# Optimization experiments

Measured on AMD Instinct MI355X. Metric: run time of the kernel, lower is better.

## Reference

```python
import jax, jax.numpy as jnp
import numpy as np

B, N, F_IN, F_OUT, T, K = 2, 4096, 16, 16, 12, 3


def setup_inputs() -> dict:
    key = jax.random.key(0)
    k1, k2, k3, k4 = jax.random.split(key, 4)
    x = jax.random.normal(k1, (B, N, F_IN, T), dtype=jnp.float32)
    # stacked K Chebyshev polynomial matrices T_k(L~), each (N, N)
    cheb_polynomials = jax.random.normal(k2, (K, N, N), dtype=jnp.float32) / np.sqrt(N)
    # ChebNetII interpolation table: cheb_poly_xj[j, k] = T_k evaluated at node x_j (scalar)
    cheb_poly_xj = jax.random.normal(k3, (K, K), dtype=jnp.float32)
    # learned Gamma_j parameters, each (F_in, F_out)
    Gamma = jax.random.normal(k4, (K, F_IN, F_OUT), dtype=jnp.float32) * 0.1
    return {"x": x, "cheb_polynomials": cheb_polynomials,
            "cheb_poly_xj": cheb_poly_xj, "Gamma": Gamma}


def reference(x, cheb_polynomials, cheb_poly_xj, Gamma):
    # x: (B, N, F_in, T); cheb_polynomials: (K, N, N);
    # cheb_poly_xj: (K, K) scalars; Gamma: (K, F_in, F_out)
    K_ = Gamma.shape[0]
    # lhs_k = sum_j Gamma_j * cheb_poly_xj[j, k]  -> (K, F_in, F_out); hoisted out of T loop
    lhs = jnp.einsum('jio,jk->kio', Gamma, cheb_poly_xj)
    # project features first (small contraction): (K, B, N, F_out, T)
    z = jnp.einsum('bmft,kfo->kbmot', x, lhs)
    # graph propagation: rhs[b,n,f] = sum_m x[b,m,f] * T_k[m, n]  (note T_k applied on the right)
    out = jnp.einsum('kmn,kbmot->bnot', cheb_polynomials, z)
    return jax.nn.relu((2.0 / (K_ + 1)) * out)
```

## Files before the change

### kernel.cpp

```cpp
#include <hip/hip_runtime.h>
#include <stdint.h>

typedef float    f32x2 __attribute__((ext_vector_type(2)));
typedef float    f32x4 __attribute__((ext_vector_type(4)));
typedef _Float16 f16x8 __attribute__((ext_vector_type(8)));
typedef unsigned int u32x4 __attribute__((ext_vector_type(4)));

#define NN     4096
#define KTOT   12288
#define CDIM   384
#define BN     64
#define BK     32
#define TSTEPS 384

__global__ __launch_bounds__(256) void zbuild_kernel(
    const float* __restrict__ x,
    const float* __restrict__ xj,
    const float* __restrict__ gamma,
    _Float16* __restrict__ zws)
{
  __shared__ float xs[32 * 193];
  __shared__ float lhs[768];
  const int tid = threadIdx.x;
  const int b   = blockIdx.x & 1;
  const int m0  = (blockIdx.x >> 1) << 5;

  for (int e = tid; e < 768; e += 256) {
    const int k = e >> 8, fo = e & 255;
    float s = 0.f;
#pragma unroll
    for (int j = 0; j < 3; ++j) s += gamma[j * 256 + fo] * xj[j * 3 + k];
    lhs[e] = s;
  }
  const float* xsrc = x + (size_t)(b * 4096 + m0) * 192;
  for (int q = tid; q < 1536; q += 256) {
    const int fl  = q << 2;
    const int ml  = fl / 192;
    const int off = fl - ml * 192;
    const f32x4 v = *(const f32x4*)(xsrc + fl);
#pragma unroll
    for (int r = 0; r < 4; ++r) xs[ml * 193 + off + r] = v[r];
  }
  __syncthreads();

  for (int slot = tid; slot < 512; slot += 256) {
    const int ml = slot & 31, o = slot >> 5;
    float acc[3][12];
#pragma unroll
    for (int k = 0; k < 3; ++k)
#pragma unroll
      for (int t = 0; t < 12; ++t) acc[k][t] = 0.f;

#pragma unroll
    for (int f = 0; f < 16; ++f) {
      float xv[12];
#pragma unroll
      for (int t = 0; t < 12; ++t) xv[t] = xs[ml * 193 + f * 12 + t];
#pragma unroll
      for (int k = 0; k < 3; ++k) {
        const float lf = lhs[k * 256 + f * 16 + o];
#pragma unroll
        for (int t = 0; t < 12; ++t) acc[k][t] += xv[t] * lf;
      }
    }
    const int mg = m0 + ml;
    const int cb = b * 192 + o * 12;
#pragma unroll
    for (int k = 0; k < 3; ++k)
#pragma unroll
      for (int t = 0; t < 12; ++t)
        zws[(size_t)(cb + t) * KTOT + k * 4096 + mg] = (_Float16)acc[k][t];
  }
}

__global__ __launch_bounds__(512, 4) void gemm_kernel(
    const float* __restrict__ cheb,
    const _Float16* __restrict__ zws,
    float* __restrict__ partials,
    int S, int spb)
{
  __shared__ unsigned int Bs[2][BN * BK / 2];

  const int tid  = threadIdx.x;
  const int by   = blockIdx.x % S;
  const int bx   = blockIdx.x / S;
  const int lane = tid & 63, wid = tid >> 6;
  const int l15  = lane & 15, l4 = lane >> 4;
  const int nbase = bx * BN;
  const int step0 = by * spb;
  int nsteps = TSTEPS - step0;
  if (nsteps > spb) nsteps = spb;
  if (nsteps < 0) nsteps = 0;

  f32x4 acc[3][4];
#pragma unroll
  for (int mi = 0; mi < 3; ++mi)
#pragma unroll
    for (int ni = 0; ni < 4; ++ni) acc[mi][ni] = (f32x4)(0.f);

  const int rr = tid >> 5;
  const int nn = (tid & 31) << 1;
  f32x2 b0, b1;
  auto LOADB = [&](int t) {
    const float* base = cheb + (size_t)(step0 + t) * BK * NN + nbase + nn;
    b0 = *(const f32x2*)(base + (size_t)(2 * rr)     * NN);
    b1 = *(const f32x2*)(base + (size_t)(2 * rr + 1) * NN);
  };
  auto WRITEB = [&](int buf) {
#pragma unroll
    for (int d = 0; d < 2; ++d) {
      const int n = nn + d;
      const _Float16 h0 = (_Float16)b0[d], h1 = (_Float16)b1[d];
      const uint32_t w = (uint32_t)__builtin_bit_cast(unsigned short, h0) |
                         ((uint32_t)__builtin_bit_cast(unsigned short, h1) << 16);
      const int blk = (n * 4 + (rr >> 2)) ^ ((n >> 2) & 3);
      Bs[buf][blk * 4 + (rr & 3)] = w;
    }
  };

  const char* abase = (const char*)zws +
      (size_t)(wid * 48 + l15) * (KTOT * 2) + (size_t)l4 * 16;
  auto LOADA = [&](int t, u32x4* ar) {
    const size_t kb = (size_t)(step0 + t) * (BK * 2);
#pragma unroll
    for (int mi = 0; mi < 3; ++mi)
      ar[mi] = *(const u32x4*)(abase + (size_t)mi * 16 * (KTOT * 2) + kb);
  };

  auto STEP = [&](int t, u32x4* arCur, u32x4* arNxt, int cur) {
    const bool pf = (t + 1 < nsteps);
    if (pf) LOADB(t + 1);
    f16x8 bf[4];
#pragma unroll
    for (int ni = 0; ni < 4; ++ni) {
      const int n   = ni * 16 + l15;
      const int blk = (n * 4 + l4) ^ ((n >> 2) & 3);
      bf[ni] = *(const f16x8*)&Bs[cur][blk * 4];
    }
    if (pf) LOADA(t + 1, arNxt);
#pragma unroll
    for (int mi = 0; mi < 3; ++mi) {
      const f16x8 af = __builtin_bit_cast(f16x8, arCur[mi]);
#pragma unroll
      for (int ni = 0; ni < 4; ++ni)
        acc[mi][ni] = __builtin_amdgcn_mfma_f32_16x16x32_f16(
            af, bf[ni], acc[mi][ni], 0, 0, 0);
    }
    if (pf) WRITEB(cur ^ 1);
    __syncthreads();
  };

  u32x4 arA[3], arB[3];
  if (nsteps > 0) {
    LOADB(0); WRITEB(0); LOADA(0, arA);
    __syncthreads();
    int t = 0;
    for (; t + 1 < nsteps; t += 2) {
      STEP(t,     arA, arB, t & 1);
      STEP(t + 1, arB, arA, (t + 1) & 1);
    }
    if (t < nsteps) STEP(t, arA, arB, t & 1);
  }

  float* pb = partials + (size_t)by * ((size_t)CDIM * NN);
#pragma unroll
  for (int mi = 0; mi < 3; ++mi) {
    const int c0 = wid * 48 + mi * 16 + l4 * 4;
#pragma unroll
    for (int ni = 0; ni < 4; ++ni) {
      const int n = nbase + ni * 16 + l15;
#pragma unroll
      for (int r = 0; r < 4; ++r)
        pb[(size_t)(c0 + r) * NN + n] = acc[mi][ni][r];
    }
  }
}

__global__ __launch_bounds__(256) void reduce_kernel(
    const float* __restrict__ partials, float* __restrict__ out, int S)
{
  __shared__ float T[192 * 33];
  const int tid = threadIdx.x;
  const int n0  = blockIdx.x * 32;
  const int cb  = blockIdx.y;

  for (int i = tid; i < 6144; i += 256) {
    const int c_l = i >> 5, n_l = i & 31;
    const float* p = partials + (size_t)(cb * 192 + c_l) * NN + n0 + n_l;
    float s = 0.f;
    for (int ss = 0; ss < S; ++ss) s += p[(size_t)ss * ((size_t)CDIM * NN)];
    T[c_l * 33 + n_l] = s;
  }
  __syncthreads();
  for (int j = tid; j < 6144; j += 256) {
    const int n_l = j / 192, ot = j - n_l * 192;
    const float v = 0.5f * T[ot * 33 + n_l];
    out[(size_t)(cb * 4096 + n0 + n_l) * 192 + ot] = v > 0.f ? v : 0.f;
  }
}

extern "C" void kernel_launch(void* const* d_in, const int* in_sizes, int n_in,
                              void* d_out, int out_size, void* d_ws, size_t ws_size,
                              hipStream_t stream) {
  (void)in_sizes; (void)n_in; (void)out_size;
  const float* x     = (const float*)d_in[0];
  const float* cheb  = (const float*)d_in[1];
  const float* xj    = (const float*)d_in[2];
  const float* gamma = (const float*)d_in[3];
  float* out = (float*)d_out;

  const long long zbytes = (long long)CDIM * KTOT * 2;
  const long long pslab  = (long long)CDIM * NN * 4;
  int S = 8;
  const long long avail = (long long)ws_size - zbytes;
  if (avail < 8 * pslab) {
    S = (int)(avail / pslab);
    if (S < 1) S = 1;
    if (S > 8) S = 8;
  }
  const int spb = (TSTEPS + S - 1) / S;

  _Float16* zws   = (_Float16*)d_ws;
  float* partials = (float*)((char*)d_ws + zbytes);

  zbuild_kernel<<<256, 256, 0, stream>>>(x, xj, gamma, zws);
  gemm_kernel<<<(NN / BN) * S, 512, 0, stream>>>(cheb, zws, partials, S, spb);
  reduce_kernel<<<dim3(128, 2), 256, 0, stream>>>(partials, out, S);
}
```

Measured before the change: 413.8 us.

## Deepen global prefetch to two steps and use lighter LDS-only barrier

The B tile (cheb) global loads are now issued two steps ahead using two rotating register buffers, while A still prefetches one step ahead. The __syncthreads is replaced by an explicit lgkmcnt wait plus s_barrier, so outstanding global loads (vmcnt) need not drain at each step. The LDS swizzle XOR changes from (n>>2)&3 to (n>>1)&7 to reduce bank conflicts. The aim is to hide HBM latency of the streamed fp32 matrix, at the cost of extra registers and reliance on the compiler's vmcnt handling for correctness.

```diff
diff --git a/kernel.cpp b/kernel.cpp
--- a/kernel.cpp
+++ b/kernel.cpp
@@ -100,20 +100,20 @@
 
   const int rr = tid >> 5;
   const int nn = (tid & 31) << 1;
-  f32x2 b0, b1;
-  auto LOADB = [&](int t) {
+  auto LOADB = [&](int t, f32x2* br) {
     const float* base = cheb + (size_t)(step0 + t) * BK * NN + nbase + nn;
-    b0 = *(const f32x2*)(base + (size_t)(2 * rr)     * NN);
-    b1 = *(const f32x2*)(base + (size_t)(2 * rr + 1) * NN);
-  };
-  auto WRITEB = [&](int buf) {
+    br[0] = *(const f32x2*)(base + (size_t)(2 * rr)     * NN);
+    br[1] = *(const f32x2*)(base + (size_t)(2 * rr + 1) * NN);
+  };
+  auto WRITEB = [&](int buf, f32x2* br) {
 #pragma unroll
     for (int d = 0; d < 2; ++d) {
       const int n = nn + d;
-      const _Float16 h0 = (_Float16)b0[d], h1 = (_Float16)b1[d];
+      const _Float16 h0 = (_Float16)br[0][d];
+      const _Float16 h1 = (_Float16)br[1][d];
       const uint32_t w = (uint32_t)__builtin_bit_cast(unsigned short, h0) |
                          ((uint32_t)__builtin_bit_cast(unsigned short, h1) << 16);
-      const int blk = (n * 4 + (rr >> 2)) ^ ((n >> 2) & 3);
+      const int blk = (n * 4 + (rr >> 2)) ^ ((n >> 1) & 7);
       Bs[buf][blk * 4 + (rr & 3)] = w;
     }
   };
@@ -127,39 +127,44 @@
       ar[mi] = *(const u32x4*)(abase + (size_t)mi * 16 * (KTOT * 2) + kb);
   };
 
-  auto STEP = [&](int t, u32x4* arCur, u32x4* arNxt, int cur) {
-    const bool pf = (t + 1 < nsteps);
-    if (pf) LOADB(t + 1);
+  auto STEP = [&](int t, int cur, f32x2* bL, f32x2* bW, u32x4* arC, u32x4* arN) {
+    if (t + 1 < nsteps) LOADA(t + 1, arN);
+    if (t + 2 < nsteps) LOADB(t + 2, bL);
     f16x8 bf[4];
 #pragma unroll
     for (int ni = 0; ni < 4; ++ni) {
       const int n   = ni * 16 + l15;
-      const int blk = (n * 4 + l4) ^ ((n >> 2) & 3);
+      const int blk = (n * 4 + l4) ^ ((n >> 1) & 7);
       bf[ni] = *(const f16x8*)&Bs[cur][blk * 4];
     }
-    if (pf) LOADA(t + 1, arNxt);
 #pragma unroll
     for (int mi = 0; mi < 3; ++mi) {
-      const f16x8 af = __builtin_bit_cast(f16x8, arCur[mi]);
+      const f16x8 af = __builtin_bit_cast(f16x8, arC[mi]);
 #pragma unroll
       for (int ni = 0; ni < 4; ++ni)
         acc[mi][ni] = __builtin_amdgcn_mfma_f32_16x16x32_f16(
             af, bf[ni], acc[mi][ni], 0, 0, 0);
     }
-    if (pf) WRITEB(cur ^ 1);
-    __syncthreads();
-  };
-
+    if (t + 1 < nsteps) WRITEB(cur ^ 1, bW);
+    asm volatile("s_waitcnt lgkmcnt(0)" ::: "memory");
+    __builtin_amdgcn_s_barrier();
+  };
+
+  f32x2 bs0[2], bs1[2];
   u32x4 arA[3], arB[3];
   if (nsteps > 0) {
-    LOADB(0); WRITEB(0); LOADA(0, arA);
-    __syncthreads();
+    LOADA(0, arA);
+    LOADB(0, bs0);
+    if (nsteps > 1) LOADB(1, bs1);
+    WRITEB(0, bs0);
+    asm volatile("s_waitcnt lgkmcnt(0)" ::: "memory");
+    __builtin_amdgcn_s_barrier();
     int t = 0;
     for (; t + 1 < nsteps; t += 2) {
-      STEP(t,     arA, arB, t & 1);
-      STEP(t + 1, arB, arA, (t + 1) & 1);
-    }
-    if (t < nsteps) STEP(t, arA, arB, t & 1);
+      STEP(t,     0, bs0, bs1, arA, arB);
+      STEP(t + 1, 1, bs1, bs0, arB, arA);
+    }
+    if (t < nsteps) STEP(t, 0, bs0, bs1, arA, arB);
   }
 
   float* pb = partials + (size_t)by * ((size_t)CDIM * NN);
```

Measured after the change: 411.6 us. About the same (-0.5%).

## Deepen GEMM prefetch pipeline and change LDS swizzle with manual barriers

Applied to the files above, without the earlier changes.

The GEMM main loop is rewritten with macros to prefetch the cheb (B) tiles four steps ahead and the z (A) fragments two steps ahead in rotating register sets. Each phase now writes the next LDS buffer before the MFMAs instead of after them. The LDS XOR swizzle changes from ((n>>2)&3) to ((n>>1)&7) to reduce bank conflicts. The __syncthreads is replaced by an explicit lgkmcnt wait plus s_barrier. The aim is to hide global-memory latency behind the MFMAs, at the cost of more registers under a 512-thread launch bound that allows 4 blocks.

```diff
diff --git a/kernel.cpp b/kernel.cpp
--- a/kernel.cpp
+++ b/kernel.cpp
@@ -73,6 +73,56 @@
   }
 }
 
+#define LOADA_(T, R0, R1, R2) do {                                          \
+    const size_t kb_ = (size_t)(step0 + (T)) * (BK * 2);                    \
+    R0 = *(const u32x4*)(abase + kb_);                                      \
+    R1 = *(const u32x4*)(abase + (size_t)16 * (KTOT * 2) + kb_);            \
+    R2 = *(const u32x4*)(abase + (size_t)32 * (KTOT * 2) + kb_);            \
+  } while (0)
+
+#define LOADB_(T, QA, QB) do {                                              \
+    const float* base_ = cheb + (size_t)(step0 + (T)) * BK * NN + nbase + nn; \
+    QA = *(const f32x2*)(base_ + (size_t)(2 * rr) * NN);                    \
+    QB = *(const f32x2*)(base_ + (size_t)(2 * rr + 1) * NN);                \
+  } while (0)
+
+#define WRITEB_(BUF, QA, QB) do {                                           \
+    _Float16 h0_, h1_; uint32_t w_;                                         \
+    h0_ = (_Float16)QA[0]; h1_ = (_Float16)QB[0];                           \
+    w_ = (uint32_t)__builtin_bit_cast(unsigned short, h0_) |                \
+         ((uint32_t)__builtin_bit_cast(unsigned short, h1_) << 16);         \
+    Bs[BUF][(((nn) * 4 + (rr >> 2)) ^ (((nn) >> 1) & 7)) * 4 + (rr & 3)] = w_; \
+    h0_ = (_Float16)QA[1]; h1_ = (_Float16)QB[1];                           \
+    w_ = (uint32_t)__builtin_bit_cast(unsigned short, h0_) |                \
+         ((uint32_t)__builtin_bit_cast(unsigned short, h1_) << 16);         \
+    Bs[BUF][(((nn + 1) * 4 + (rr >> 2)) ^ (((nn + 1) >> 1) & 7)) * 4 + (rr & 3)] = w_; \
+  } while (0)
+
+#define MFMA_ROW_(MI, AREG)                                                 \
+  { const f16x8 af_ = __builtin_bit_cast(f16x8, AREG);                      \
+    acc[MI][0] = __builtin_amdgcn_mfma_f32_16x16x32_f16(af_, bf0_, acc[MI][0], 0, 0, 0); \
+    acc[MI][1] = __builtin_amdgcn_mfma_f32_16x16x32_f16(af_, bf1_, acc[MI][1], 0, 0, 0); \
+    acc[MI][2] = __builtin_amdgcn_mfma_f32_16x16x32_f16(af_, bf2_, acc[MI][2], 0, 0, 0); \
+    acc[MI][3] = __builtin_amdgcn_mfma_f32_16x16x32_f16(af_, bf3_, acc[MI][3], 0, 0, 0); }
+
+#define PHASE_(T, A0_, A1_, A2_, QWA, QWB, QLA, QLB) do {                   \
+    const int t_ = (T);                                                     \
+    const int cur_ = t_ & 1;                                                \
+    f16x8 bf0_, bf1_, bf2_, bf3_;                                           \
+    { const int n_ = l15;      bf0_ = *(const f16x8*)&Bs[cur_][((n_ * 4 + l4) ^ ((n_ >> 1) & 7)) * 4]; } \
+    { const int n_ = 16 + l15; bf1_ = *(const f16x8*)&Bs[cur_][((n_ * 4 + l4) ^ ((n_ >> 1) & 7)) * 4]; } \
+    { const int n_ = 32 + l15; bf2_ = *(const f16x8*)&Bs[cur_][((n_ * 4 + l4) ^ ((n_ >> 1) & 7)) * 4]; } \
+    { const int n_ = 48 + l15; bf3_ = *(const f16x8*)&Bs[cur_][((n_ * 4 + l4) ^ ((n_ >> 1) & 7)) * 4]; } \
+    if (t_ + 1 < nsteps) WRITEB_((t_ + 1) & 1, QWA, QWB);                   \
+    MFMA_ROW_(0, A0_)                                                       \
+    MFMA_ROW_(1, A1_)                                                       \
+    MFMA_ROW_(2, A2_)                                                       \
+    if (t_ + 2 < nsteps) LOADA_(t_ + 2, A0_, A1_, A2_);                     \
+    if (t_ + 4 < nsteps) LOADB_(t_ + 4, QLA, QLB);                          \
+    asm volatile("s_waitcnt lgkmcnt(0)" ::: "memory");                      \
+    __builtin_amdgcn_s_barrier();                                           \
+  } while (0)
+
 __global__ __launch_bounds__(512, 4) void gemm_kernel(
     const float* __restrict__ cheb,
     const _Float16* __restrict__ zws,
@@ -100,66 +150,29 @@
 
   const int rr = tid >> 5;
   const int nn = (tid & 31) << 1;
-  f32x2 b0, b1;
-  auto LOADB = [&](int t) {
-    const float* base = cheb + (size_t)(step0 + t) * BK * NN + nbase + nn;
-    b0 = *(const f32x2*)(base + (size_t)(2 * rr)     * NN);
-    b1 = *(const f32x2*)(base + (size_t)(2 * rr + 1) * NN);
-  };
-  auto WRITEB = [&](int buf) {
-#pragma unroll
-    for (int d = 0; d < 2; ++d) {
-      const int n = nn + d;
-      const _Float16 h0 = (_Float16)b0[d], h1 = (_Float16)b1[d];
-      const uint32_t w = (uint32_t)__builtin_bit_cast(unsigned short, h0) |
-                         ((uint32_t)__builtin_bit_cast(unsigned short, h1) << 16);
-      const int blk = (n * 4 + (rr >> 2)) ^ ((n >> 2) & 3);
-      Bs[buf][blk * 4 + (rr & 3)] = w;
-    }
-  };
 
   const char* abase = (const char*)zws +
       (size_t)(wid * 48 + l15) * (KTOT * 2) + (size_t)l4 * 16;
-  auto LOADA = [&](int t, u32x4* ar) {
-    const size_t kb = (size_t)(step0 + t) * (BK * 2);
-#pragma unroll
-    for (int mi = 0; mi < 3; ++mi)
-      ar[mi] = *(const u32x4*)(abase + (size_t)mi * 16 * (KTOT * 2) + kb);
-  };
-
-  auto STEP = [&](int t, u32x4* arCur, u32x4* arNxt, int cur) {
-    const bool pf = (t + 1 < nsteps);
-    if (pf) LOADB(t + 1);
-    f16x8 bf[4];
-#pragma unroll
-    for (int ni = 0; ni < 4; ++ni) {
-      const int n   = ni * 16 + l15;
-      const int blk = (n * 4 + l4) ^ ((n >> 2) & 3);
-      bf[ni] = *(const f16x8*)&Bs[cur][blk * 4];
+
+  u32x4 A00, A01, A02, A10, A11, A12;
+  f32x2 q0a, q0b, q1a, q1b, q2a, q2b, q3a, q3b;
+
+  if (nsteps > 0) {
+    LOADA_(0, A00, A01, A02);
+    if (nsteps > 1) LOADA_(1, A10, A11, A12);
+    LOADB_(0, q0a, q0b);
+    if (nsteps > 1) LOADB_(1, q1a, q1b);
+    if (nsteps > 2) LOADB_(2, q2a, q2b);
+    if (nsteps > 3) LOADB_(3, q3a, q3b);
+    WRITEB_(0, q0a, q0b);
+    asm volatile("s_waitcnt lgkmcnt(0)" ::: "memory");
+    __builtin_amdgcn_s_barrier();
+    for (int t = 0; t < nsteps; t += 4) {
+      PHASE_(t + 0, A00, A01, A02, q1a, q1b, q0a, q0b);
+      if (t + 1 < nsteps) PHASE_(t + 1, A10, A11, A12, q2a, q2b, q1a, q1b);
+      if (t + 2 < nsteps) PHASE_(t + 2, A00, A01, A02, q3a, q3b, q2a, q2b);
+      if (t + 3 < nsteps) PHASE_(t + 3, A10, A11, A12, q0a, q0b, q3a, q3b);
     }
-    if (pf) LOADA(t + 1, arNxt);
-#pragma unroll
-    for (int mi = 0; mi < 3; ++mi) {
-      const f16x8 af = __builtin_bit_cast(f16x8, arCur[mi]);
-#pragma unroll
-      for (int ni = 0; ni < 4; ++ni)
-        acc[mi][ni] = __builtin_amdgcn_mfma_f32_16x16x32_f16(
-            af, bf[ni], acc[mi][ni], 0, 0, 0);
-    }
-    if (pf) WRITEB(cur ^ 1);
-    __syncthreads();
-  };
-
-  u32x4 arA[3], arB[3];
-  if (nsteps > 0) {
-    LOADB(0); WRITEB(0); LOADA(0, arA);
-    __syncthreads();
-    int t = 0;
-    for (; t + 1 < nsteps; t += 2) {
-      STEP(t,     arA, arB, t & 1);
-      STEP(t + 1, arB, arA, (t + 1) & 1);
-    }
-    if (t < nsteps) STEP(t, arA, arB, t & 1);
   }
 
   float* pb = partials + (size_t)by * ((size_t)CDIM * NN);
```

Result: no change. 411.5 us (-0.6%).
